# Performance work log

Hardware: AMD Instinct MI355X
Metric: run time of the kernel (lower is better)

## Reference

```python
import jax, jax.numpy as jnp
import numpy as np
from jax import lax

# 19 edges over 19 body-joint heatmap channels (0..18); PAF channels are 19..56
EDGES = np.array([[1,8],[8,9],[9,10],[1,11],[11,12],[12,13],[1,2],[2,3],[3,4],[2,16],
                  [1,5],[5,6],[6,7],[5,17],[0,1],[0,14],[0,15],[14,16],[15,17]], dtype=np.int32)
_i = np.arange(19, dtype=np.int32)
# per-edge 4 input channels: [node_a, node_b, paf_x(=19+2i), paf_y(=20+2i)]
CH_IDX = np.concatenate([EDGES, (19 + 2*_i)[:, None], (20 + 2*_i)[:, None]], axis=1)  # [19,4]

_W_SHAPES = [(16,4,5,5),(16,16,5,5),(32,16,5,5),(32,32,5,5),(32,32,5,5),(128,32,1,1),(2,128,1,1)]

def _conv(x, w, b):
    p = (w.shape[-1] - 1) // 2  # padding=2 for 5x5, 0 for 1x1
    y = lax.conv_general_dilated(x, w, window_strides=(1,1), padding=[(p,p),(p,p)],
                                 dimension_numbers=('NCHW','OIHW','NCHW'))
    return y + b[None, :, None, None]

def setup_inputs() -> dict:
    key = jax.random.key(0)
    keys = jax.random.split(key, 1 + 2*len(_W_SHAPES))
    N, C, H, W = 16, 57, 128, 128
    inp = {'cnn_output': jax.random.normal(keys[0], (N, C, H, W), dtype=jnp.float32),
           'gnn_interations': 1}
    for i, s in enumerate(_W_SHAPES):
        inp[f'w{i}'] = jax.random.normal(keys[1+2*i], s, dtype=jnp.float32) * 0.01
        inp[f'b{i}'] = jax.random.normal(keys[2+2*i], (s[0],), dtype=jnp.float32) * 0.01
    return inp

def reference(cnn_output, gnn_interations, w0, b0, w1, b1, w2, b2, w3, b3, w4, b4, w5, b5, w6, b6):
    N, _, H, Wd = cnn_output.shape
    ws = (w0, w1, w2, w3, w4, w5, w6)
    bs = (b0, b1, b2, b3, b4, b5, b6)
    # gather per-edge 4-channel inputs: [N,19,4,H,W] -> fold edges into batch
    x = cnn_output[:, jnp.asarray(CH_IDX)]            # [N,19,4,H,W]
    x = x.reshape(N * 19, 4, H, Wd)
    for i in range(7):
        x = _conv(x, ws[i], bs[i])
        if i != 6:
            x = jax.nn.relu(x)
    # edge n output (2 ch) -> output channels [2n, 2n+1]
    return x.reshape(N, 38, H, Wd)
```

## Files before the change

### kernel.cpp

```cpp
#include <hip/hip_runtime.h>
#include <hip/hip_bf16.h>

typedef __bf16  bf16x8 __attribute__((ext_vector_type(8)));
typedef float   f32x4  __attribute__((ext_vector_type(4)));

__device__ __constant__ int EDGE_A[19] = {1,8,9,1,11,12,1,2,3,2,1,5,6,5,0,0,0,14,15};
__device__ __constant__ int EDGE_B[19] = {8,9,10,11,12,13,2,3,4,16,5,6,7,17,1,14,15,16,17};

#define SACT  64.0f
#define SINV  (1.0f / 4096.0f)
#define SREQ  0.015625f

__device__ __forceinline__ unsigned short f2bf(float f) {
    unsigned int x = __float_as_uint(f);
    x += 0x7FFFu + ((x >> 16) & 1u);
    return (unsigned short)(x >> 16);
}
__device__ __forceinline__ unsigned int pack2(float a, float b) {
    __hip_bfloat162 t = __float22bfloat162_rn(make_float2(a, b));
    unsigned int r; __builtin_memcpy(&r, &t, 4); return r;
}
__device__ __forceinline__ unsigned char f2fp8(float v) {
    int r = __builtin_amdgcn_cvt_pk_fp8_f32(v, 0.f, 0, false);
    return (unsigned char)(r & 0xff);
}
__device__ __forceinline__ unsigned int pk4fp8(float a, float b, float c, float d) {
    int v = __builtin_amdgcn_cvt_pk_fp8_f32(a, b, 0, false);
    v = __builtin_amdgcn_cvt_pk_fp8_f32(c, d, v, true);
    return (unsigned int)v;
}
__device__ __forceinline__ unsigned int quant4(f32x4 a, float4 b, float s, bool oob) {
    float v0 = fmaxf(fmaf(a[0], s, b.x), 0.f);
    float v1 = fmaxf(fmaf(a[1], s, b.y), 0.f);
    float v2 = fmaxf(fmaf(a[2], s, b.z), 0.f);
    float v3 = fmaxf(fmaf(a[3], s, b.w), 0.f);
    unsigned int v = pk4fp8(v0, v1, v2, v3);
    return oob ? 0u : v;
}

__device__ __forceinline__ int sw8 (int l) { return l ^ ((l >> 4) & 8);  }
__device__ __forceinline__ int sw32(int l) { return l ^ ((l >> 5) & 24); }
__device__ __forceinline__ int sw48(int l) { return l ^ ((l >> 3) & 48); }

__device__ __forceinline__ void store_relu4(unsigned char* dst, f32x4 a, float4 b, bool oob) {
    unsigned int lo = pack2(fmaxf(a[0] + b.x, 0.f), fmaxf(a[1] + b.y, 0.f));
    unsigned int hi = pack2(fmaxf(a[2] + b.z, 0.f), fmaxf(a[3] + b.w, 0.f));
    uint2 v; v.x = oob ? 0u : lo; v.y = oob ? 0u : hi;
    *(uint2*)dst = v;
}

extern "C" __global__ void __launch_bounds__(256)
reorder_weights(const float* __restrict__ w0, const float* __restrict__ w1,
                const float* __restrict__ w2, const float* __restrict__ w3,
                const float* __restrict__ w4, const float* __restrict__ w5,
                unsigned char* __restrict__ ws)
{
    int idx = blockIdx.x * 256 + threadIdx.x;
    unsigned short* wsS = (unsigned short*)ws;
    if (idx < 4096) {
        int k = idx & 31, oc = idx >> 5;
        wsS[idx] = f2bf(w5[oc * 32 + k]);
    } else if (idx < 6144) {
        int j = idx - 4096;
        int k = j & 31, n = (j >> 5) & 15, c = j >> 9;
        int t = c * 8 + (k >> 2), ic = k & 3;
        float v = (t < 25) ? w0[(n * 4 + ic) * 25 + t] : 0.f;
        wsS[idx] = f2bf(v);
    }
    if (idx < 6656) {
        int k = idx & 31, n = (idx >> 5) & 15, tp = idx >> 9;
        int t = 2 * tp + (k >> 4), ic = k & 15;
        float v = (t < 25) ? w1[(n * 16 + ic) * 25 + t] * SACT : 0.f;
        ws[12288 + idx] = f2fp8(v);
    } else if (idx < 19968) {
        int j = idx - 6656;
        int k = j & 31, n = (j >> 5) & 15, nt = (j >> 9) & 1, tp = j >> 10;
        int t = 2 * tp + (k >> 4), ic = k & 15, oc = nt * 16 + n;
        float v = (t < 25) ? w2[(oc * 16 + ic) * 25 + t] * SACT : 0.f;
        ws[18944 + j] = f2fp8(v);
    } else if (idx < 45568) {
        int j = idx - 19968;
        int k = j & 31, n = (j >> 5) & 15, nt = (j >> 9) & 1, tap = j >> 10;
        ws[32256 + j] = f2fp8(w3[((nt * 16 + n) * 32 + k) * 25 + tap] * SACT);
    } else if (idx < 71168) {
        int j = idx - 45568;
        int k = j & 31, n = (j >> 5) & 15, nt = (j >> 9) & 1, tap = j >> 10;
        ws[57856 + j] = f2fp8(w4[((nt * 16 + n) * 32 + k) * 25 + tap] * SACT);
    }
}

__device__ __forceinline__ void conv0_slab(
    const unsigned short* __restrict__ s_in, unsigned char* __restrict__ s0,
    const unsigned char* __restrict__ wB, const float* __restrict__ b0,
    int yoff, int oy, int ox, int wave, int lane)
{
    const int nl = lane & 15, quad = lane >> 4;
    const unsigned short* w0p = (const unsigned short*)(wB + 8192);
    bf16x8 wf[4];
#pragma unroll
    for (int c = 0; c < 4; ++c)
        wf[c] = *(const bf16x8*)(w0p + c * 512 + nl * 32 + quad * 8);
    float4 bb = *(const float4*)(b0 + quad * 4);
    float4 bbs = make_float4(bb.x * SACT, bb.y * SACT, bb.z * SACT, bb.w * SACT);
#pragma unroll 1
    for (int i = 0; i < 9; ++i) {
        int mt = wave + 4 * i;
        int p = mt * 16 + nl;
        int y = p >> 5, x = p & 31;
        f32x4 acc = (f32x4)0.f;
#pragma unroll
        for (int c = 0; c < 4; ++c) {
            int t0 = c * 8 + quad * 2, t1 = t0 + 1;
            if (t0 > 24) t0 = 24;
            if (t1 > 24) t1 = 24;
            int dy0 = t0 / 5, dx0 = t0 - 5 * dy0;
            int dy1 = t1 / 5, dx1 = t1 - 5 * dy1;
            uint2 lo = *(const uint2*)(s_in + ((y + dy0) * 36 + x + dx0) * 4);
            uint2 hi = *(const uint2*)(s_in + ((y + dy1) * 36 + x + dx1) * 4);
            bf16x8 a;
            ((uint2*)&a)[0] = lo; ((uint2*)&a)[1] = hi;
            acc = __builtin_amdgcn_mfma_f32_16x16x32_bf16(wf[c], a, acc, 0, 0, 0);
        }
        bool oob = ((unsigned)(oy - 8 + y + yoff) >= 128u) || ((unsigned)(ox - 8 + x) >= 128u);
        *(unsigned int*)(s0 + sw8(p * 16 + quad * 4)) = quant4(acc, bbs, SACT, oob);
    }
}

__device__ __forceinline__ void conv1_fp8(
    const unsigned char* __restrict__ s0, unsigned char* __restrict__ s1,
    const unsigned char* __restrict__ wB, const float* __restrict__ b1,
    int POFF, int gy0, int gx0, int wave, int lane)
{
    const int nl = lane & 15, quad = lane >> 4;
    const int h = quad >> 1, g8 = (quad & 1) * 8;

    int abase[7];
#pragma unroll
    for (int i = 0; i < 7; ++i) {
        int p = (wave + 4 * i) * 16 + nl;
        if (p > 391) p = 391;
        int y = p / 28, x = p - y * 28;
        abase[i] = (y * 32 + x) * 16 + g8;
    }
    f32x4 acc[7];
#pragma unroll
    for (int i = 0; i < 7; ++i) acc[i] = (f32x4)0.f;

    const unsigned char* wp = wB + 12288 + nl * 32 + quad * 8;

#pragma unroll 1
    for (int c0 = 0; c0 < 13; c0 += 5) {
        long wl[5];
#pragma unroll
        for (int tp = 0; tp < 5; ++tp)
            if (c0 + tp < 13) wl[tp] = *(const long*)(wp + (c0 + tp) * 512);
#pragma unroll
        for (int tp = 0; tp < 5; ++tp) {
            if (c0 + tp < 13) {
                int t = 2 * (c0 + tp) + h;
                if (t > 24) t = 24;
                int dy = t / 5, dx = t - 5 * dy;
                int toff = (dy * 32 + dx) * 16;
#pragma unroll
                for (int i = 0; i < 7; ++i)
                    if (wave + 4 * i < 25) {
                        long a = *(const long*)(s0 + sw8(abase[i] + toff));
                        acc[i] = __builtin_amdgcn_mfma_f32_16x16x32_fp8_fp8(wl[tp], a, acc[i], 0, 0, 0);
                    }
            }
        }
    }

    float4 bb = *(const float4*)(b1 + quad * 4);
    float4 bbs = make_float4(bb.x * SACT, bb.y * SACT, bb.z * SACT, bb.w * SACT);
#pragma unroll
    for (int i = 0; i < 7; ++i) {
        int p = (wave + 4 * i) * 16 + nl;
        if (p < 392) {
            int pg = p + POFF;
            int y = pg / 28, x = pg - y * 28;
            bool oob = ((unsigned)(gy0 + y) >= 128u) || ((unsigned)(gx0 + x) >= 128u);
            *(unsigned int*)(s1 + sw8(pg * 16 + quad * 4)) = quant4(acc[i], bbs, SREQ, oob);
        }
    }
}

template<int I0, int NI>
__device__ __forceinline__ void conv2_fp8(
    const unsigned char* __restrict__ s1, unsigned char* __restrict__ s2,
    const unsigned char* __restrict__ wA, const float* __restrict__ b2,
    int gy0, int gx0, int wave, int lane)
{
    const int nl = lane & 15, quad = lane >> 4;
    const int h = quad >> 1, g8 = (quad & 1) * 8;

    int abase[NI];
#pragma unroll
    for (int i = 0; i < NI; ++i) {
        int p = (wave + 4 * (I0 + i)) * 16 + nl;
        int y = p / 24, x = p - y * 24;
        abase[i] = (y * 28 + x) * 16 + g8;
    }
    f32x4 acc[NI][2];
#pragma unroll
    for (int i = 0; i < NI; ++i) { acc[i][0] = (f32x4)0.f; acc[i][1] = (f32x4)0.f; }

    const unsigned char* wp = wA + nl * 32 + quad * 8;

#pragma unroll 1
    for (int c0 = 0; c0 < 13; c0 += 3) {
        long wl[3][2];
#pragma unroll
        for (int tp = 0; tp < 3; ++tp)
            if (c0 + tp < 13) {
                wl[tp][0] = *(const long*)(wp + ((c0 + tp) * 2 + 0) * 512);
                wl[tp][1] = *(const long*)(wp + ((c0 + tp) * 2 + 1) * 512);
            }
#pragma unroll
        for (int tp = 0; tp < 3; ++tp) {
            if (c0 + tp < 13) {
                int t = 2 * (c0 + tp) + h;
                if (t > 24) t = 24;
                int dy = t / 5, dx = t - 5 * dy;
                int toff = (dy * 28 + dx) * 16;
#pragma unroll
                for (int i = 0; i < NI; ++i) {
                    long a = *(const long*)(s1 + sw8(abase[i] + toff));
                    acc[i][0] = __builtin_amdgcn_mfma_f32_16x16x32_fp8_fp8(wl[tp][0], a, acc[i][0], 0, 0, 0);
                    acc[i][1] = __builtin_amdgcn_mfma_f32_16x16x32_fp8_fp8(wl[tp][1], a, acc[i][1], 0, 0, 0);
                }
            }
        }
    }

#pragma unroll
    for (int i = 0; i < NI; ++i) {
        int p = (wave + 4 * (I0 + i)) * 16 + nl;
        int y = p / 24, x = p - y * 24;
        bool oob = ((unsigned)(gy0 + y) >= 128u) || ((unsigned)(gx0 + x) >= 128u);
#pragma unroll
        for (int nt = 0; nt < 2; ++nt) {
            float4 bb = *(const float4*)(b2 + nt * 16 + quad * 4);
            float4 bbs = make_float4(bb.x * SACT, bb.y * SACT, bb.z * SACT, bb.w * SACT);
            *(unsigned int*)(s2 + sw32(p * 32 + nt * 16 + quad * 4)) =
                quant4(acc[i][nt], bbs, SREQ, oob);
        }
    }
}

template<int SIN, int SOUT, int MAXM, bool GUARD, bool FP8OUT, int CH>
__device__ __forceinline__ void conv_c32_fp8(
    const unsigned char* __restrict__ sinB, unsigned char* __restrict__ soutB,
    const unsigned char* __restrict__ wA, const float* __restrict__ bias,
    int gy0, int gx0, int wave, int lane)
{
    constexpr int NM = (SOUT * SOUT) / 16;
    const int nl = lane & 15, quad = lane >> 4;

    int abase[MAXM];
#pragma unroll
    for (int i = 0; i < MAXM; ++i) {
        int p = (wave + 4 * i) * 16 + nl;
        if (GUARD && p > SOUT * SOUT - 1) p = SOUT * SOUT - 1;
        int y = p / SOUT, x = p - y * SOUT;
        abase[i] = (y * SIN + x) * 32 + quad * 8;
    }
    f32x4 acc[MAXM][2];
#pragma unroll
    for (int i = 0; i < MAXM; ++i) { acc[i][0] = (f32x4)0.f; acc[i][1] = (f32x4)0.f; }

    const unsigned char* wp = wA + nl * 32 + quad * 8;

#pragma unroll 1
    for (int c0 = 0; c0 < 25; c0 += CH) {
        long wl[CH][2];
#pragma unroll
        for (int tp = 0; tp < CH; ++tp)
            if (c0 + tp < 25) {
                wl[tp][0] = *(const long*)(wp + ((c0 + tp) * 2 + 0) * 512);
                wl[tp][1] = *(const long*)(wp + ((c0 + tp) * 2 + 1) * 512);
            }
#pragma unroll
        for (int tp = 0; tp < CH; ++tp) {
            if (c0 + tp < 25) {
                int t = c0 + tp;
                int dy = t / 5, dx = t - 5 * dy;
                int toff = (dy * SIN + dx) * 32;
#pragma unroll
                for (int i = 0; i < MAXM; ++i)
                    if (!GUARD || wave + 4 * i < NM) {
                        long a = *(const long*)(sinB + sw32(abase[i] + toff));
                        acc[i][0] = __builtin_amdgcn_mfma_f32_16x16x32_fp8_fp8(wl[tp][0], a, acc[i][0], 0, 0, 0);
                        acc[i][1] = __builtin_amdgcn_mfma_f32_16x16x32_fp8_fp8(wl[tp][1], a, acc[i][1], 0, 0, 0);
                    }
            }
        }
    }

#pragma unroll
    for (int i = 0; i < MAXM; ++i) {
        int p = (wave + 4 * i) * 16 + nl;
        if (!GUARD || p < SOUT * SOUT) {
            int y = p / SOUT, x = p - y * SOUT;
            bool oob = ((unsigned)(gy0 + y) >= 128u) || ((unsigned)(gx0 + x) >= 128u);
#pragma unroll
            for (int nt = 0; nt < 2; ++nt) {
                float4 bb = *(const float4*)(bias + nt * 16 + quad * 4);
                if (FP8OUT) {
                    float4 bbs = make_float4(bb.x * SACT, bb.y * SACT, bb.z * SACT, bb.w * SACT);
                    *(unsigned int*)(soutB + sw32(p * 32 + nt * 16 + quad * 4)) =
                        quant4(acc[i][nt], bbs, SREQ, oob);
                } else {
                    f32x4 s;
                    s[0] = acc[i][nt][0] * SINV; s[1] = acc[i][nt][1] * SINV;
                    s[2] = acc[i][nt][2] * SINV; s[3] = acc[i][nt][3] * SINV;
                    store_relu4(soutB + sw48(p * 64 + nt * 32 + quad * 8), s, bb, oob);
                }
            }
        }
    }
}

extern "C" __global__ void __launch_bounds__(256, 3)
gnn_paf_mfma(const float* __restrict__ cnn, const unsigned char* __restrict__ wB,
             const float* __restrict__ b0, const float* __restrict__ b1,
             const float* __restrict__ b2, const float* __restrict__ b3,
             const float* __restrict__ b4, const float* __restrict__ b5,
             const float* __restrict__ w6, const float* __restrict__ b6,
             float* __restrict__ out)
{
    __shared__ __align__(64) unsigned char smem[31232];
    unsigned char*  const s1   = smem;
    unsigned char*  const s3   = smem;
    unsigned short* const sin_ = (unsigned short*)(smem + 12800);
    unsigned char*  const s0   = smem + 19136;
    unsigned char*  const s2   = smem + 12800;
    unsigned char*  const s4   = smem + 12800;

    const int tid  = threadIdx.x;
    const int lane = tid & 63, wave = tid >> 6;
    const int tile = blockIdx.x, img = blockIdx.y;
    const int oy = (tile >> 3) * 16, ox = (tile & 7) * 16;
    const int n = img / 19, g = img - n * 19;
    const int ch0 = EDGE_A[g], ch1 = EDGE_B[g], ch2 = 19 + 2 * g, ch3 = 20 + 2 * g;
    const int nl = lane & 15, quad = lane >> 4;
    const long long nb = (long long)n * 57 * 16384;

    for (int idx = tid; idx < 792; idx += 256) {
        int r = idx / 36, c = idx - r * 36;
        int gy = oy - 10 + r, gx = ox - 10 + c;
        float v0 = 0.f, v1 = 0.f, v2 = 0.f, v3 = 0.f;
        if ((unsigned)gy < 128u && (unsigned)gx < 128u) {
            int off = gy * 128 + gx;
            v0 = cnn[nb + (long long)ch0 * 16384 + off];
            v1 = cnn[nb + (long long)ch1 * 16384 + off];
            v2 = cnn[nb + (long long)ch2 * 16384 + off];
            v3 = cnn[nb + (long long)ch3 * 16384 + off];
        }
        uint2 v; v.x = pack2(v0, v1); v.y = pack2(v2, v3);
        *(uint2*)(sin_ + idx * 4) = v;
    }
    __syncthreads();

    conv0_slab(sin_, s0, wB, b0, 0, oy, ox, wave, lane);
    __syncthreads();

    float gv[4][4];
#pragma unroll
    for (int j = 0; j < 4; ++j) {
        gv[j][0] = gv[j][1] = gv[j][2] = gv[j][3] = 0.f;
        int idx = tid + 256 * j;
        if (idx < 792) {
            int r = idx / 36, c = idx - r * 36;
            int gy = oy + 4 + r, gx = ox - 10 + c;
            if ((unsigned)gy < 128u && (unsigned)gx < 128u) {
                int off = gy * 128 + gx;
                gv[j][0] = cnn[nb + (long long)ch0 * 16384 + off];
                gv[j][1] = cnn[nb + (long long)ch1 * 16384 + off];
                gv[j][2] = cnn[nb + (long long)ch2 * 16384 + off];
                gv[j][3] = cnn[nb + (long long)ch3 * 16384 + off];
            }
        }
    }
    conv1_fp8(s0, s1, wB, b1, 0, oy - 6, ox - 6, wave, lane);
#pragma unroll
    for (int j = 0; j < 4; ++j) {
        int idx = tid + 256 * j;
        if (idx < 792) {
            uint2 v; v.x = pack2(gv[j][0], gv[j][1]); v.y = pack2(gv[j][2], gv[j][3]);
            *(uint2*)(sin_ + idx * 4) = v;
        }
    }
    __syncthreads();

    conv0_slab(sin_, s0, wB, b0, 14, oy, ox, wave, lane);
    __syncthreads();

    conv1_fp8(s0, s1, wB, b1, 392, oy - 6, ox - 6, wave, lane);
    __syncthreads();

    conv2_fp8<0, 5>(s1, s2, wB + 18944, b2, oy - 4, ox - 4, wave, lane);
    conv2_fp8<5, 4>(s1, s2, wB + 18944, b2, oy - 4, ox - 4, wave, lane);
    __syncthreads();

    conv_c32_fp8<24, 20, 7, true,  true,  3>(s2, s3, wB + 32256, b3, oy - 2, ox - 2, wave, lane);
    __syncthreads();

    conv_c32_fp8<20, 16, 4, false, false, 5>(s3, s4, wB + 57856, b4, oy, ox, wave, lane);
    __syncthreads();

    {
        const unsigned short* w5p = (const unsigned short*)wB;
        bf16x8 w5f[8];
#pragma unroll
        for (int nt = 0; nt < 8; ++nt)
            w5f[nt] = *(const bf16x8*)(w5p + nt * 512 + nl * 32 + quad * 8);
        const float b6q = b6[quad & 1];
#pragma unroll 1
        for (int ii = 0; ii < 4; ++ii) {
            int mt = wave + 4 * ii;
            int lin = (mt * 16 + nl) * 64 + quad * 16;
            bf16x8 pf = *(const bf16x8*)(s4 + sw48(lin));
            float o0 = 0.f, o1 = 0.f;
#pragma unroll
            for (int nt = 0; nt < 8; ++nt) {
                f32x4 acc = (f32x4)0.f;
                acc = __builtin_amdgcn_mfma_f32_16x16x32_bf16(w5f[nt], pf, acc, 0, 0, 0);
                float4 bb  = *(const float4*)(b5 + nt * 16 + quad * 4);
                float4 wa  = *(const float4*)(w6 + nt * 16 + quad * 4);
                float4 wb2 = *(const float4*)(w6 + 128 + nt * 16 + quad * 4);
                float h0 = fmaxf(acc[0] + bb.x, 0.f), h1 = fmaxf(acc[1] + bb.y, 0.f);
                float h2 = fmaxf(acc[2] + bb.z, 0.f), h3 = fmaxf(acc[3] + bb.w, 0.f);
                o0 = fmaf(h0, wa.x, fmaf(h1, wa.y, fmaf(h2, wa.z, fmaf(h3, wa.w, o0))));
                o1 = fmaf(h0, wb2.x, fmaf(h1, wb2.y, fmaf(h2, wb2.z, fmaf(h3, wb2.w, o1))));
            }
            o0 += __shfl_xor(o0, 16, 64); o0 += __shfl_xor(o0, 32, 64);
            o1 += __shfl_xor(o1, 16, 64); o1 += __shfl_xor(o1, 32, 64);
            if (quad < 2) {
                float val = ((quad == 0) ? o0 : o1) + b6q;
                long long ob = (((long long)n * 38 + 2 * g + quad) * 128 + (oy + mt)) * 128 + (ox + nl);
                out[ob] = val;
            }
        }
    }
}

extern "C" void kernel_launch(void* const* d_in, const int* in_sizes, int n_in,
                              void* d_out, int out_size, void* d_ws, size_t ws_size,
                              hipStream_t stream) {
    const float* cnn = (const float*)d_in[0];
    const float* w0 = (const float*)d_in[2];  const float* b0 = (const float*)d_in[3];
    const float* w1 = (const float*)d_in[4];  const float* b1 = (const float*)d_in[5];
    const float* w2 = (const float*)d_in[6];  const float* b2 = (const float*)d_in[7];
    const float* w3 = (const float*)d_in[8];  const float* b3 = (const float*)d_in[9];
    const float* w4 = (const float*)d_in[10]; const float* b4 = (const float*)d_in[11];
    const float* w5 = (const float*)d_in[12]; const float* b5 = (const float*)d_in[13];
    const float* w6 = (const float*)d_in[14]; const float* b6 = (const float*)d_in[15];
    float* out = (float*)d_out;
    unsigned char* wB = (unsigned char*)d_ws;

    hipLaunchKernelGGL(reorder_weights, dim3(278), dim3(256), 0, stream,
                       w0, w1, w2, w3, w4, w5, wB);
    hipLaunchKernelGGL(gnn_paf_mfma, dim3(64, 304), dim3(256), 0, stream,
                       cnn, wB, b0, b1, b2, b3, b4, b5, w6, b6, out);
}
```

Baseline: 1.248 ms.

## Switch LDS activations to 16-byte channel-plane layout and fully unroll tap loops

Replaces the XOR-swizzled interleaved LDS activation layouts with planar layouts, where each 16-byte channel group of a pixel lives in its own plane (9216/6400/4096-byte strides). Every conv stage reads and writes these planes. The swizzle arithmetic is removed, and the tap offsets become compile-time constants, so the conv0/conv1/conv2 tap loops are now fully unrolled with precomputed offsets. This cuts address computation and lets the compiler schedule the loads. The risks are bank conflicts now that the swizzle is gone, higher register pressure from full unrolling under launch bounds of 3 blocks, and possible plane overlap in the shared buffer.

```diff
diff --git a/kernel.cpp b/kernel.cpp
--- a/kernel.cpp
+++ b/kernel.cpp
@@ -10,6 +10,11 @@
 #define SACT  64.0f
 #define SINV  (1.0f / 4096.0f)
 #define SREQ  0.015625f
+
+__device__ constexpr int ctoff(int t, int sin, int gr) {
+    int tt = t > 24 ? 24 : t;
+    return ((tt / 5) * sin + (tt % 5)) * gr;
+}
 
 __device__ __forceinline__ unsigned short f2bf(float f) {
     unsigned int x = __float_as_uint(f);
@@ -37,10 +42,6 @@
     unsigned int v = pk4fp8(v0, v1, v2, v3);
     return oob ? 0u : v;
 }
-
-__device__ __forceinline__ int sw8 (int l) { return l ^ ((l >> 4) & 8);  }
-__device__ __forceinline__ int sw32(int l) { return l ^ ((l >> 5) & 24); }
-__device__ __forceinline__ int sw48(int l) { return l ^ ((l >> 3) & 48); }
 
 __device__ __forceinline__ void store_relu4(unsigned char* dst, f32x4 a, float4 b, bool oob) {
     unsigned int lo = pack2(fmaxf(a[0] + b.x, 0.f), fmaxf(a[1] + b.y, 0.f));
@@ -102,27 +103,35 @@
         wf[c] = *(const bf16x8*)(w0p + c * 512 + nl * 32 + quad * 8);
     float4 bb = *(const float4*)(b0 + quad * 4);
     float4 bbs = make_float4(bb.x * SACT, bb.y * SACT, bb.z * SACT, bb.w * SACT);
+
+    int coff0[4], coff1[4];
+#pragma unroll
+    for (int c = 0; c < 4; ++c) {
+        int t0 = c * 8 + quad * 2, t1 = t0 + 1;
+        if (t0 > 24) t0 = 24;
+        if (t1 > 24) t1 = 24;
+        coff0[c] = ((t0 / 5) * 36 + (t0 % 5)) * 8;
+        coff1[c] = ((t1 / 5) * 36 + (t1 % 5)) * 8;
+    }
+    const unsigned char* sB = (const unsigned char*)s_in;
+
 #pragma unroll 1
     for (int i = 0; i < 9; ++i) {
         int mt = wave + 4 * i;
         int p = mt * 16 + nl;
         int y = p >> 5, x = p & 31;
+        int abase = (y * 36 + x) * 8;
         f32x4 acc = (f32x4)0.f;
 #pragma unroll
         for (int c = 0; c < 4; ++c) {
-            int t0 = c * 8 + quad * 2, t1 = t0 + 1;
-            if (t0 > 24) t0 = 24;
-            if (t1 > 24) t1 = 24;
-            int dy0 = t0 / 5, dx0 = t0 - 5 * dy0;
-            int dy1 = t1 / 5, dx1 = t1 - 5 * dy1;
-            uint2 lo = *(const uint2*)(s_in + ((y + dy0) * 36 + x + dx0) * 4);
-            uint2 hi = *(const uint2*)(s_in + ((y + dy1) * 36 + x + dx1) * 4);
+            uint2 lo = *(const uint2*)(sB + abase + coff0[c]);
+            uint2 hi = *(const uint2*)(sB + abase + coff1[c]);
             bf16x8 a;
             ((uint2*)&a)[0] = lo; ((uint2*)&a)[1] = hi;
             acc = __builtin_amdgcn_mfma_f32_16x16x32_bf16(wf[c], a, acc, 0, 0, 0);
         }
         bool oob = ((unsigned)(oy - 8 + y + yoff) >= 128u) || ((unsigned)(ox - 8 + x) >= 128u);
-        *(unsigned int*)(s0 + sw8(p * 16 + quad * 4)) = quant4(acc, bbs, SACT, oob);
+        *(unsigned int*)(s0 + p * 16 + quad * 4) = quant4(acc, bbs, SACT, oob);
     }
 }
 
@@ -148,27 +157,16 @@
 
     const unsigned char* wp = wB + 12288 + nl * 32 + quad * 8;
 
-#pragma unroll 1
-    for (int c0 = 0; c0 < 13; c0 += 5) {
-        long wl[5];
-#pragma unroll
-        for (int tp = 0; tp < 5; ++tp)
-            if (c0 + tp < 13) wl[tp] = *(const long*)(wp + (c0 + tp) * 512);
-#pragma unroll
-        for (int tp = 0; tp < 5; ++tp) {
-            if (c0 + tp < 13) {
-                int t = 2 * (c0 + tp) + h;
-                if (t > 24) t = 24;
-                int dy = t / 5, dx = t - 5 * dy;
-                int toff = (dy * 32 + dx) * 16;
-#pragma unroll
-                for (int i = 0; i < 7; ++i)
-                    if (wave + 4 * i < 25) {
-                        long a = *(const long*)(s0 + sw8(abase[i] + toff));
-                        acc[i] = __builtin_amdgcn_mfma_f32_16x16x32_fp8_fp8(wl[tp], a, acc[i], 0, 0, 0);
-                    }
-            }
-        }
+#pragma unroll
+    for (int tp = 0; tp < 13; ++tp) {
+        long wl = *(const long*)(wp + tp * 512);
+        int to = h ? ctoff(2 * tp + 1, 32, 16) : ctoff(2 * tp, 32, 16);
+#pragma unroll
+        for (int i = 0; i < 7; ++i)
+            if (wave + 4 * i < 25) {
+                long a = *(const long*)(s0 + abase[i] + to);
+                acc[i] = __builtin_amdgcn_mfma_f32_16x16x32_fp8_fp8(wl, a, acc[i], 0, 0, 0);
+            }
     }
 
     float4 bb = *(const float4*)(b1 + quad * 4);
@@ -180,7 +178,7 @@
             int pg = p + POFF;
             int y = pg / 28, x = pg - y * 28;
             bool oob = ((unsigned)(gy0 + y) >= 128u) || ((unsigned)(gx0 + x) >= 128u);
-            *(unsigned int*)(s1 + sw8(pg * 16 + quad * 4)) = quant4(acc[i], bbs, SREQ, oob);
+            *(unsigned int*)(s1 + pg * 16 + quad * 4) = quant4(acc[i], bbs, SREQ, oob);
         }
     }
 }
@@ -207,29 +205,16 @@
 
     const unsigned char* wp = wA + nl * 32 + quad * 8;
 
-#pragma unroll 1
-    for (int c0 = 0; c0 < 13; c0 += 3) {
-        long wl[3][2];
-#pragma unroll
-        for (int tp = 0; tp < 3; ++tp)
-            if (c0 + tp < 13) {
-                wl[tp][0] = *(const long*)(wp + ((c0 + tp) * 2 + 0) * 512);
-                wl[tp][1] = *(const long*)(wp + ((c0 + tp) * 2 + 1) * 512);
-            }
-#pragma unroll
-        for (int tp = 0; tp < 3; ++tp) {
-            if (c0 + tp < 13) {
-                int t = 2 * (c0 + tp) + h;
-                if (t > 24) t = 24;
-                int dy = t / 5, dx = t - 5 * dy;
-                int toff = (dy * 28 + dx) * 16;
-#pragma unroll
-                for (int i = 0; i < NI; ++i) {
-                    long a = *(const long*)(s1 + sw8(abase[i] + toff));
-                    acc[i][0] = __builtin_amdgcn_mfma_f32_16x16x32_fp8_fp8(wl[tp][0], a, acc[i][0], 0, 0, 0);
-                    acc[i][1] = __builtin_amdgcn_mfma_f32_16x16x32_fp8_fp8(wl[tp][1], a, acc[i][1], 0, 0, 0);
-                }
-            }
+#pragma unroll
+    for (int tp = 0; tp < 13; ++tp) {
+        long wl0 = *(const long*)(wp + (tp * 2 + 0) * 512);
+        long wl1 = *(const long*)(wp + (tp * 2 + 1) * 512);
+        int to = h ? ctoff(2 * tp + 1, 28, 16) : ctoff(2 * tp, 28, 16);
+#pragma unroll
+        for (int i = 0; i < NI; ++i) {
+            long a = *(const long*)(s1 + abase[i] + to);
+            acc[i][0] = __builtin_amdgcn_mfma_f32_16x16x32_fp8_fp8(wl0, a, acc[i][0], 0, 0, 0);
+            acc[i][1] = __builtin_amdgcn_mfma_f32_16x16x32_fp8_fp8(wl1, a, acc[i][1], 0, 0, 0);
         }
     }
 
@@ -242,13 +227,14 @@
         for (int nt = 0; nt < 2; ++nt) {
             float4 bb = *(const float4*)(b2 + nt * 16 + quad * 4);
             float4 bbs = make_float4(bb.x * SACT, bb.y * SACT, bb.z * SACT, bb.w * SACT);
-            *(unsigned int*)(s2 + sw32(p * 32 + nt * 16 + quad * 4)) =
+            *(unsigned int*)(s2 + nt * 9216 + p * 16 + quad * 4) =
                 quant4(acc[i][nt], bbs, SREQ, oob);
         }
     }
 }
 
-template<int SIN, int SOUT, int MAXM, bool GUARD, bool FP8OUT, int CH>
+template<int SIN, int SOUT, int MAXM, bool GUARD, bool FP8OUT, int CH,
+         int PLANE_IN, int PLANE_OUT>
 __device__ __forceinline__ void conv_c32_fp8(
     const unsigned char* __restrict__ sinB, unsigned char* __restrict__ soutB,
     const unsigned char* __restrict__ wA, const float* __restrict__ bias,
@@ -263,7 +249,7 @@
         int p = (wave + 4 * i) * 16 + nl;
         if (GUARD && p > SOUT * SOUT - 1) p = SOUT * SOUT - 1;
         int y = p / SOUT, x = p - y * SOUT;
-        abase[i] = (y * SIN + x) * 32 + quad * 8;
+        abase[i] = (y * SIN + x) * 16 + (quad & 1) * 8 + (quad >> 1) * PLANE_IN;
     }
     f32x4 acc[MAXM][2];
 #pragma unroll
@@ -285,11 +271,11 @@
             if (c0 + tp < 25) {
                 int t = c0 + tp;
                 int dy = t / 5, dx = t - 5 * dy;
-                int toff = (dy * SIN + dx) * 32;
+                int to = (dy * SIN + dx) * 16;
 #pragma unroll
                 for (int i = 0; i < MAXM; ++i)
                     if (!GUARD || wave + 4 * i < NM) {
-                        long a = *(const long*)(sinB + sw32(abase[i] + toff));
+                        long a = *(const long*)(sinB + abase[i] + to);
                         acc[i][0] = __builtin_amdgcn_mfma_f32_16x16x32_fp8_fp8(wl[tp][0], a, acc[i][0], 0, 0, 0);
                         acc[i][1] = __builtin_amdgcn_mfma_f32_16x16x32_fp8_fp8(wl[tp][1], a, acc[i][1], 0, 0, 0);
                     }
@@ -308,13 +294,14 @@
                 float4 bb = *(const float4*)(bias + nt * 16 + quad * 4);
                 if (FP8OUT) {
                     float4 bbs = make_float4(bb.x * SACT, bb.y * SACT, bb.z * SACT, bb.w * SACT);
-                    *(unsigned int*)(soutB + sw32(p * 32 + nt * 16 + quad * 4)) =
+                    *(unsigned int*)(soutB + nt * PLANE_OUT + p * 16 + quad * 4) =
                         quant4(acc[i][nt], bbs, SREQ, oob);
                 } else {
                     f32x4 s;
                     s[0] = acc[i][nt][0] * SINV; s[1] = acc[i][nt][1] * SINV;
                     s[2] = acc[i][nt][2] * SINV; s[3] = acc[i][nt][3] * SINV;
-                    store_relu4(soutB + sw48(p * 64 + nt * 32 + quad * 8), s, bb, oob);
+                    store_relu4(soutB + (2 * nt + (quad >> 1)) * PLANE_OUT
+                                      + p * 16 + (quad & 1) * 8, s, bb, oob);
                 }
             }
         }
@@ -403,10 +390,10 @@
     conv2_fp8<5, 4>(s1, s2, wB + 18944, b2, oy - 4, ox - 4, wave, lane);
     __syncthreads();
 
-    conv_c32_fp8<24, 20, 7, true,  true,  3>(s2, s3, wB + 32256, b3, oy - 2, ox - 2, wave, lane);
-    __syncthreads();
-
-    conv_c32_fp8<20, 16, 4, false, false, 5>(s3, s4, wB + 57856, b4, oy, ox, wave, lane);
+    conv_c32_fp8<24, 20, 7, true,  true,  3, 9216, 6400>(s2, s3, wB + 32256, b3, oy - 2, ox - 2, wave, lane);
+    __syncthreads();
+
+    conv_c32_fp8<20, 16, 4, false, false, 5, 6400, 4096>(s3, s4, wB + 57856, b4, oy, ox, wave, lane);
     __syncthreads();
 
     {
@@ -419,8 +406,8 @@
 #pragma unroll 1
         for (int ii = 0; ii < 4; ++ii) {
             int mt = wave + 4 * ii;
-            int lin = (mt * 16 + nl) * 64 + quad * 16;
-            bf16x8 pf = *(const bf16x8*)(s4 + sw48(lin));
+            int lin = (mt * 16 + nl) * 16 + quad * 4096;
+            bf16x8 pf = *(const bf16x8*)(s4 + lin);
             float o0 = 0.f, o1 = 0.f;
 #pragma unroll
             for (int nt = 0; nt < 8; ++nt) {
```

New measurement: 2.444 ms. 1.96x slower.

## Use 16x16x128 scaled FP8 MFMA for 32-channel 5x5 convs with padded layout

Applied to the files above, without the earlier changes.

Switches conv3 and conv4 from 16x16x32 fp8 MFMAs (one tap per instruction) to MI355 block-scaled 16x16x128 f8f6f4 MFMAs. Each instruction now covers four taps, with unit scales and the 25 taps padded to 28. The weights are reordered into tap groups of four, and the activation layout is padded to a 48-byte pixel stride without swizzle so each lane can load 32 contiguous bytes. This raises LDS use from about 31KB to 47KB, which may reduce occupancy, and adds wasted work on the padded taps. It also precomputes the conv0 tap offsets outside the loop.

```diff
diff --git a/kernel.cpp b/kernel.cpp
--- a/kernel.cpp
+++ b/kernel.cpp
@@ -3,6 +3,8 @@
 
 typedef __bf16  bf16x8 __attribute__((ext_vector_type(8)));
 typedef float   f32x4  __attribute__((ext_vector_type(4)));
+typedef int     i32x4  __attribute__((ext_vector_type(4)));
+typedef int     i32x8  __attribute__((ext_vector_type(8)));
 
 __device__ __constant__ int EDGE_A[19] = {1,8,9,1,11,12,1,2,3,2,1,5,6,5,0,0,0,14,15};
 __device__ __constant__ int EDGE_B[19] = {8,9,10,11,12,13,2,3,4,16,5,6,7,17,1,14,15,16,17};
@@ -10,6 +12,7 @@
 #define SACT  64.0f
 #define SINV  (1.0f / 4096.0f)
 #define SREQ  0.015625f
+#define SCL1  0x7F7F7F7F
 
 __device__ __forceinline__ unsigned short f2bf(float f) {
     unsigned int x = __float_as_uint(f);
@@ -39,7 +42,6 @@
 }
 
 __device__ __forceinline__ int sw8 (int l) { return l ^ ((l >> 4) & 8);  }
-__device__ __forceinline__ int sw32(int l) { return l ^ ((l >> 5) & 24); }
 __device__ __forceinline__ int sw48(int l) { return l ^ ((l >> 3) & 48); }
 
 __device__ __forceinline__ void store_relu4(unsigned char* dst, f32x4 a, float4 b, bool oob) {
@@ -78,14 +80,20 @@
         int t = 2 * tp + (k >> 4), ic = k & 15, oc = nt * 16 + n;
         float v = (t < 25) ? w2[(oc * 16 + ic) * 25 + t] * SACT : 0.f;
         ws[18944 + j] = f2fp8(v);
-    } else if (idx < 45568) {
+    } else if (idx < 48640) {
         int j = idx - 19968;
-        int k = j & 31, n = (j >> 5) & 15, nt = (j >> 9) & 1, tap = j >> 10;
-        ws[32256 + j] = f2fp8(w3[((nt * 16 + n) * 32 + k) * 25 + tap] * SACT);
-    } else if (idx < 71168) {
-        int j = idx - 45568;
-        int k = j & 31, n = (j >> 5) & 15, nt = (j >> 9) & 1, tap = j >> 10;
-        ws[57856 + j] = f2fp8(w4[((nt * 16 + n) * 32 + k) * 25 + tap] * SACT);
+        int tg = j >> 12, r = j & 4095;
+        int nt = r >> 11, n = (r >> 7) & 15, q = (r >> 5) & 3, ic = r & 31;
+        int tap = 4 * tg + q;
+        float v = (tap < 25) ? w3[((nt * 16 + n) * 32 + ic) * 25 + tap] * SACT : 0.f;
+        ws[32256 + j] = f2fp8(v);
+    } else if (idx < 77312) {
+        int j = idx - 48640;
+        int tg = j >> 12, r = j & 4095;
+        int nt = r >> 11, n = (r >> 7) & 15, q = (r >> 5) & 3, ic = r & 31;
+        int tap = 4 * tg + q;
+        float v = (tap < 25) ? w4[((nt * 16 + n) * 32 + ic) * 25 + tap] * SACT : 0.f;
+        ws[60928 + j] = f2fp8(v);
     }
 }
 
@@ -102,21 +110,29 @@
         wf[c] = *(const bf16x8*)(w0p + c * 512 + nl * 32 + quad * 8);
     float4 bb = *(const float4*)(b0 + quad * 4);
     float4 bbs = make_float4(bb.x * SACT, bb.y * SACT, bb.z * SACT, bb.w * SACT);
+
+    int coff0[4], coff1[4];
+#pragma unroll
+    for (int c = 0; c < 4; ++c) {
+        int t0 = c * 8 + quad * 2, t1 = t0 + 1;
+        if (t0 > 24) t0 = 24;
+        if (t1 > 24) t1 = 24;
+        coff0[c] = ((t0 / 5) * 36 + (t0 % 5)) * 8;
+        coff1[c] = ((t1 / 5) * 36 + (t1 % 5)) * 8;
+    }
+    const unsigned char* sB = (const unsigned char*)s_in;
+
 #pragma unroll 1
     for (int i = 0; i < 9; ++i) {
         int mt = wave + 4 * i;
         int p = mt * 16 + nl;
         int y = p >> 5, x = p & 31;
+        int abase = (y * 36 + x) * 8;
         f32x4 acc = (f32x4)0.f;
 #pragma unroll
         for (int c = 0; c < 4; ++c) {
-            int t0 = c * 8 + quad * 2, t1 = t0 + 1;
-            if (t0 > 24) t0 = 24;
-            if (t1 > 24) t1 = 24;
-            int dy0 = t0 / 5, dx0 = t0 - 5 * dy0;
-            int dy1 = t1 / 5, dx1 = t1 - 5 * dy1;
-            uint2 lo = *(const uint2*)(s_in + ((y + dy0) * 36 + x + dx0) * 4);
-            uint2 hi = *(const uint2*)(s_in + ((y + dy1) * 36 + x + dx1) * 4);
+            uint2 lo = *(const uint2*)(sB + abase + coff0[c]);
+            uint2 hi = *(const uint2*)(sB + abase + coff1[c]);
             bf16x8 a;
             ((uint2*)&a)[0] = lo; ((uint2*)&a)[1] = hi;
             acc = __builtin_amdgcn_mfma_f32_16x16x32_bf16(wf[c], a, acc, 0, 0, 0);
@@ -242,14 +258,14 @@
         for (int nt = 0; nt < 2; ++nt) {
             float4 bb = *(const float4*)(b2 + nt * 16 + quad * 4);
             float4 bbs = make_float4(bb.x * SACT, bb.y * SACT, bb.z * SACT, bb.w * SACT);
-            *(unsigned int*)(s2 + sw32(p * 32 + nt * 16 + quad * 4)) =
+            *(unsigned int*)(s2 + p * 48 + nt * 16 + quad * 4) =
                 quant4(acc[i][nt], bbs, SREQ, oob);
         }
     }
 }
 
-template<int SIN, int SOUT, int MAXM, bool GUARD, bool FP8OUT, int CH>
-__device__ __forceinline__ void conv_c32_fp8(
+template<int SINW, int SOUT, int MAXM, bool GUARD, bool FP8OUT>
+__device__ __forceinline__ void conv_c32_mx(
     const unsigned char* __restrict__ sinB, unsigned char* __restrict__ soutB,
     const unsigned char* __restrict__ wA, const float* __restrict__ bias,
     int gy0, int gx0, int wave, int lane)
@@ -263,38 +279,34 @@
         int p = (wave + 4 * i) * 16 + nl;
         if (GUARD && p > SOUT * SOUT - 1) p = SOUT * SOUT - 1;
         int y = p / SOUT, x = p - y * SOUT;
-        abase[i] = (y * SIN + x) * 32 + quad * 8;
+        abase[i] = (y * SINW + x) * 48;
     }
     f32x4 acc[MAXM][2];
 #pragma unroll
     for (int i = 0; i < MAXM; ++i) { acc[i][0] = (f32x4)0.f; acc[i][1] = (f32x4)0.f; }
 
-    const unsigned char* wp = wA + nl * 32 + quad * 8;
+    const unsigned char* wp = wA + nl * 128 + quad * 32;
 
 #pragma unroll 1
-    for (int c0 = 0; c0 < 25; c0 += CH) {
-        long wl[CH][2];
-#pragma unroll
-        for (int tp = 0; tp < CH; ++tp)
-            if (c0 + tp < 25) {
-                wl[tp][0] = *(const long*)(wp + ((c0 + tp) * 2 + 0) * 512);
-                wl[tp][1] = *(const long*)(wp + ((c0 + tp) * 2 + 1) * 512);
-            }
-#pragma unroll
-        for (int tp = 0; tp < CH; ++tp) {
-            if (c0 + tp < 25) {
-                int t = c0 + tp;
-                int dy = t / 5, dx = t - 5 * dy;
-                int toff = (dy * SIN + dx) * 32;
-#pragma unroll
-                for (int i = 0; i < MAXM; ++i)
-                    if (!GUARD || wave + 4 * i < NM) {
-                        long a = *(const long*)(sinB + sw32(abase[i] + toff));
-                        acc[i][0] = __builtin_amdgcn_mfma_f32_16x16x32_fp8_fp8(wl[tp][0], a, acc[i][0], 0, 0, 0);
-                        acc[i][1] = __builtin_amdgcn_mfma_f32_16x16x32_fp8_fp8(wl[tp][1], a, acc[i][1], 0, 0, 0);
-                    }
-            }
-        }
+    for (int tg = 0; tg < 7; ++tg) {
+        int t = 4 * tg + quad;
+        if (t > 24) t = 24;
+        int dy = t / 5, dx = t - 5 * dy;
+        int to = (dy * SINW + dx) * 48;
+        i32x8 wl0 = *(const i32x8*)(wp + tg * 4096);
+        i32x8 wl1 = *(const i32x8*)(wp + tg * 4096 + 2048);
+#pragma unroll
+        for (int i = 0; i < MAXM; ++i)
+            if (!GUARD || wave + 4 * i < NM) {
+                i32x4 alo = *(const i32x4*)(sinB + abase[i] + to);
+                i32x4 ahi = *(const i32x4*)(sinB + abase[i] + to + 16);
+                i32x8 a;
+                ((i32x4*)&a)[0] = alo; ((i32x4*)&a)[1] = ahi;
+                acc[i][0] = __builtin_amdgcn_mfma_scale_f32_16x16x128_f8f6f4(
+                                wl0, a, acc[i][0], 0, 0, 0, SCL1, 0, SCL1);
+                acc[i][1] = __builtin_amdgcn_mfma_scale_f32_16x16x128_f8f6f4(
+                                wl1, a, acc[i][1], 0, 0, 0, SCL1, 0, SCL1);
+            }
     }
 
 #pragma unroll
@@ -308,7 +320,7 @@
                 float4 bb = *(const float4*)(bias + nt * 16 + quad * 4);
                 if (FP8OUT) {
                     float4 bbs = make_float4(bb.x * SACT, bb.y * SACT, bb.z * SACT, bb.w * SACT);
-                    *(unsigned int*)(soutB + sw32(p * 32 + nt * 16 + quad * 4)) =
+                    *(unsigned int*)(soutB + p * 48 + nt * 16 + quad * 4) =
                         quant4(acc[i][nt], bbs, SREQ, oob);
                 } else {
                     f32x4 s;
@@ -329,13 +341,13 @@
              const float* __restrict__ w6, const float* __restrict__ b6,
              float* __restrict__ out)
 {
-    __shared__ __align__(64) unsigned char smem[31232];
+    __shared__ __align__(64) unsigned char smem[46848];
     unsigned char*  const s1   = smem;
     unsigned char*  const s3   = smem;
-    unsigned short* const sin_ = (unsigned short*)(smem + 12800);
-    unsigned char*  const s0   = smem + 19136;
-    unsigned char*  const s2   = smem + 12800;
-    unsigned char*  const s4   = smem + 12800;
+    unsigned short* const sin_ = (unsigned short*)(smem + 12544);
+    unsigned char*  const s0   = smem + 19200;
+    unsigned char*  const s2   = smem + 19200;
+    unsigned char*  const s4   = smem + 19200;
 
     const int tid  = threadIdx.x;
     const int lane = tid & 63, wave = tid >> 6;
@@ -403,10 +415,10 @@
     conv2_fp8<5, 4>(s1, s2, wB + 18944, b2, oy - 4, ox - 4, wave, lane);
     __syncthreads();
 
-    conv_c32_fp8<24, 20, 7, true,  true,  3>(s2, s3, wB + 32256, b3, oy - 2, ox - 2, wave, lane);
-    __syncthreads();
-
-    conv_c32_fp8<20, 16, 4, false, false, 5>(s3, s4, wB + 57856, b4, oy, ox, wave, lane);
+    conv_c32_mx<24, 20, 7, true,  true >(s2, s3, wB + 32256, b3, oy - 2, ox - 2, wave, lane);
+    __syncthreads();
+
+    conv_c32_mx<20, 16, 4, false, false>(s3, s4, wB + 60928, b4, oy, ox, wave, lane);
     __syncthreads();
 
     {
@@ -459,7 +471,7 @@
     float* out = (float*)d_out;
     unsigned char* wB = (unsigned char*)d_ws;
 
-    hipLaunchKernelGGL(reorder_weights, dim3(278), dim3(256), 0, stream,
+    hipLaunchKernelGGL(reorder_weights, dim3(302), dim3(256), 0, stream,
                        w0, w1, w2, w3, w4, w5, wB);
     hipLaunchKernelGGL(gnn_paf_mfma, dim3(64, 304), dim3(256), 0, stream,
                        cnn, wB, b0, b1, b2, b3, b4, b5, w6, b6, out);
```

New measurement: 1.170 ms (median of 2 runs). -6.2%, faster.
